# Optimization experiments

Hardware: AMD Instinct MI355X
Metric: run time of the kernel (lower is better)

The kernel has to match this reference:

```python
import jax, jax.numpy as jnp
import numpy as np

N_OPS = 8
TEMP = 1.0
EXP_CLIP = 10.0
EPS = 1e-6
# mask so that the 'none' primitive contributes exactly zero (including its bias term)
BIAS_MASK = jnp.array([0., 1., 1., 1., 1., 1., 1., 1.], dtype=jnp.float32)


def prim_feats(x):
    # x: [B, n_in] -> [B, n_in, K] primitive features
    # protected exp/ln/reciprocal to keep values finite (matches linear_clamp intent in fit())
    return jnp.stack([
        jnp.zeros_like(x),                      # none
        x,                                      # linear
        x * x,                                  # power_two
        x * x * x,                              # power_three
        jnp.exp(jnp.clip(x, -EXP_CLIP, EXP_CLIP)),  # exp
        jnp.log(jnp.abs(x) + EPS),              # ln
        x / (x * x + EPS),                      # reciprocal
        jnp.sin(x),                             # sin
    ], axis=-1)


def darts_layer(x, alphas, scale, bias):
    # alphas/scale/bias: [n_in, n_out, K]; x: [B, n_in]
    w = jax.nn.softmax(alphas / TEMP, axis=-1)          # softmax gating per (i,j)
    feats = prim_feats(x)                               # [B, n_in, K]
    out = jnp.einsum('bik,ijk->bj', feats, w * scale)   # gated sum over inputs and ops
    out = out + jnp.sum(w * bias * BIAS_MASK, axis=(0, 2))
    return out


def setup_inputs() -> dict:
    key = jax.random.key(0)
    ks = jax.random.split(key, 10)
    B, d0, d1, d2, dout, K = 16384, 512, 512, 512, 256, N_OPS
    ir, cs = 0.001, 0.1  # alpha init_range, coefficient scale
    x = jax.random.uniform(ks[0], (B, d0), dtype=jnp.float32) * 2.0 + 0.5
    alphas0 = ir * jax.random.normal(ks[1], (d0, d1, K), dtype=jnp.float32)
    scale0 = cs * jax.random.normal(ks[2], (d0, d1, K), dtype=jnp.float32)
    bias0 = cs * jax.random.normal(ks[3], (d0, d1, K), dtype=jnp.float32)
    alphas1 = ir * jax.random.normal(ks[4], (d1, d2, K), dtype=jnp.float32)
    scale1 = cs * jax.random.normal(ks[5], (d1, d2, K), dtype=jnp.float32)
    bias1 = cs * jax.random.normal(ks[6], (d1, d2, K), dtype=jnp.float32)
    W = jax.random.normal(ks[7], (dout, d2), dtype=jnp.float32) * (1.0 / np.sqrt(d2))
    b = jax.random.normal(ks[8], (dout, 1), dtype=jnp.float32) * 0.01
    return {"x": x, "alphas0": alphas0, "scale0": scale0, "bias0": bias0,
            "alphas1": alphas1, "scale1": scale1, "bias1": bias1, "W": W, "b": b}


def reference(x, alphas0, scale0, bias0, alphas1, scale1, bias1, W, b):
    h = darts_layer(x, alphas0, scale0, bias0)   # [B, 512]
    h = darts_layer(h, alphas1, scale1, bias1)   # [B, 512]
    out = h @ W.T + b.T                          # LinearDARTSLayer: [B, 256]
    return out
```

## Files before the change

### kernel.cpp

```cpp
#include <hip/hip_runtime.h>
#include <string.h>

typedef _Float16 f16x8 __attribute__((ext_vector_type(8)));
typedef float f32x4 __attribute__((ext_vector_type(4)));

#define EXP_CLIP 10.0f
#define FEPS 1e-6f
#define WSCALE 16384.0f
#define WDESCALE (1.0f/16384.0f)
#define PSCALE 1024.0f
#define PDESCALE (1.0f/1024.0f)

__device__ __forceinline__ _Float16 cvh(float v) {
  v = fminf(fmaxf(v, -60000.f), 60000.f);
  return (_Float16)v;
}

__device__ __forceinline__ void gload_lds16(const void* g, void* l) {
  __builtin_amdgcn_global_load_lds(
      (const __attribute__((address_space(1))) void*)g,
      (__attribute__((address_space(3))) void*)l, 16, 0, 0);
}

__device__ __forceinline__ int swz(int row, int colh) {
  return row * 64 + (colh ^ ((row & 7) << 3));
}

__device__ __forceinline__ float prim_eval(int kp, float x) {
  switch (kp) {
    case 0: return x;
    case 1: return x * x;
    case 2: return x * x * x;
    case 3: return __expf(fminf(fmaxf(x, -EXP_CLIP), EXP_CLIP));
    case 4: return __logf(fabsf(x) + FEPS);
    case 5: return x / (x * x + FEPS);
    default: return __sinf(x);
  }
}

__device__ __forceinline__ unsigned char enc_e5m2(float lo) {
  _Float16 lh = (_Float16)lo;
  unsigned short u;
  memcpy(&u, &lh, 2);
  unsigned t = (unsigned)u + 0x7Fu + ((u >> 8) & 1u);
  return (unsigned char)(t >> 8);
}

#define PIPE_TAIL() do { \
  __builtin_amdgcn_sched_barrier(0); \
  asm volatile("s_waitcnt vmcnt(0)" ::: "memory"); \
  __builtin_amdgcn_s_barrier(); \
  __builtin_amdgcn_sched_barrier(0); \
} while (0)

template <bool EMIT_LO>
__global__ __launch_bounds__(512)
void prep_weights(const float* __restrict__ alphas, const float* __restrict__ scale,
                  const float* __restrict__ bias, _Float16* __restrict__ Wh,
                  _Float16* __restrict__ Wl, float* __restrict__ biasvec) {
  int j = blockIdx.x;
  int i = threadIdx.x;
  size_t base = ((size_t)i * 512 + j) * 8;
  float a[8];
#pragma unroll
  for (int k = 0; k < 8; ++k) a[k] = alphas[base + k];
  float m = a[0];
#pragma unroll
  for (int k = 1; k < 8; ++k) m = fmaxf(m, a[k]);
  float e[8], sum = 0.f;
#pragma unroll
  for (int k = 0; k < 8; ++k) { e[k] = __expf(a[k] - m); sum += e[k]; }
  float inv = 1.f / sum;
  float bp = 0.f;
#pragma unroll
  for (int k = 1; k < 8; ++k) {
    float w = e[k] * inv;
    float ws = fminf(fmaxf(w * scale[base + k] * WSCALE, -60000.f), 60000.f);
    _Float16 wh = (_Float16)ws;
    size_t o = (size_t)j * 3584 + (size_t)(k - 1) * 512 + i;
    Wh[o] = wh;
    if (EMIT_LO) Wl[o] = (_Float16)(ws - (float)wh);
    bp += w * bias[base + k];
  }
  __shared__ float red[512];
  red[i] = bp;
  __syncthreads();
  for (int off = 256; off > 0; off >>= 1) {
    if (i < off) red[i] += red[i + off];
    __syncthreads();
  }
  if (i == 0) biasvec[j] = red[0];
}

__global__ __launch_bounds__(256)
void featurize_hilo(const float* __restrict__ in, _Float16* __restrict__ hi,
                    unsigned char* __restrict__ loB) {
  int t = blockIdx.x * 256 + threadIdx.x;
  int b = t >> 6, g = (t & 63) * 8;
  const float* xp = in + (size_t)b * 512 + g;
  float4 a = *(const float4*)xp;
  float4 c = *(const float4*)(xp + 4);
  float xv[8] = {a.x, a.y, a.z, a.w, c.x, c.y, c.z, c.w};
  _Float16* oh = hi + (size_t)b * 3584 + g;
  unsigned char* ol = loB + (size_t)b * 3584 + g;
#pragma unroll
  for (int kp = 0; kp < 7; ++kp) {
    f16x8 hv;
    unsigned long long lb = 0;
#pragma unroll
    for (int e = 0; e < 8; ++e) {
      float f = prim_eval(kp, xv[e]);
      _Float16 fh = (_Float16)f;
      hv[e] = fh;
      lb |= (unsigned long long)enc_e5m2(f - (float)fh) << (8 * e);
    }
    *(f16x8*)&oh[kp * 512] = hv;
    *(unsigned long long*)&ol[kp * 512] = lb;
  }
}

__global__ __launch_bounds__(256)
void featurize8(const float* __restrict__ in, _Float16* __restrict__ out) {
  int t = blockIdx.x * 256 + threadIdx.x;
  int b = t >> 6, g = (t & 63) * 8;
  const float* xp = in + (size_t)b * 512 + g;
  float4 a = *(const float4*)xp;
  float4 c = *(const float4*)(xp + 4);
  float xv[8] = {a.x, a.y, a.z, a.w, c.x, c.y, c.z, c.w};
  _Float16* o = out + (size_t)b * 3584 + g;
#pragma unroll
  for (int kp = 0; kp < 7; ++kp) {
    f16x8 v;
#pragma unroll
    for (int e = 0; e < 8; ++e) v[e] = cvh(prim_eval(kp, xv[e]));
    *(f16x8*)&o[kp * 512] = v;
  }
}

__global__ __launch_bounds__(256)
void cvt_half_k(const float* __restrict__ in, _Float16* __restrict__ out, int n) {
  int idx = blockIdx.x * 256 + threadIdx.x;
  if (idx < n) out[idx] = (_Float16)(in[idx] * PSCALE);
}

__global__ __launch_bounds__(256)
void gemm_l1_pre(const _Float16* __restrict__ Fhi, const unsigned char* __restrict__ FloB,
                 const _Float16* __restrict__ Wh, const _Float16* __restrict__ Wl,
                 const float* __restrict__ bias, float* __restrict__ H) {
  __shared__ __align__(16) _Float16 AhS[128 * 64];
  __shared__ __align__(16) unsigned char AlB[128 * 64];
  __shared__ __align__(16) _Float16 BhS[128 * 64];
  __shared__ __align__(16) _Float16 BlS[128 * 64];
  const int K = 3584;
  int lin = blockIdx.x;
  int wg = (lin & 7) * 64 + (lin >> 3);
  int bn = wg & 3, bm = wg >> 2;
  int row0 = bm * 128, col0 = bn * 128;
  int tid = threadIdx.x, lane = tid & 63, wave = tid >> 6;
  int wm = wave >> 1, wn = wave & 1;
  int l16 = lane & 15, lh = lane >> 4;
  int sr = lane >> 3, sc = ((lane & 7) * 8) ^ (sr << 3);
  int br = lane >> 2, bp_ = lane & 3;
  int bcs = (bp_ ^ ((br >> 1) & 3)) * 16;

  f32x4 acc[4][4];
#pragma unroll
  for (int m = 0; m < 4; ++m)
#pragma unroll
    for (int n = 0; n < 4; ++n) acc[m][n] = (f32x4){0.f, 0.f, 0.f, 0.f};

  for (int kk0 = 0; kk0 < K; kk0 += 64) {
    const _Float16* Agh = Fhi + (size_t)row0 * K + kk0;
    const unsigned char* Agl = FloB + (size_t)row0 * K + kk0;
    const _Float16* Bgh = Wh + (size_t)col0 * K + kk0;
    const _Float16* Bgl = Wl + (size_t)col0 * K + kk0;
#pragma unroll
    for (int it = 0; it < 4; ++it) {
      int chunk = it * 4 + wave;
      int r = chunk * 8 + sr;
      size_t go = (size_t)r * K + sc;
      gload_lds16(Agh + go, AhS + chunk * 512);
      gload_lds16(Bgh + go, BhS + chunk * 512);
      gload_lds16(Bgl + go, BlS + chunk * 512);
    }
#pragma unroll
    for (int it = 0; it < 2; ++it) {
      int chunk = it * 4 + wave;
      int r = chunk * 16 + br;
      gload_lds16(Agl + (size_t)r * K + bcs, AlB + chunk * 1024);
    }
    __syncthreads();
#pragma unroll
    for (int kc = 0; kc < 2; ++kc) {
      f16x8 ah[4], al[4];
#pragma unroll
      for (int m = 0; m < 4; ++m) {
        int row = wm * 64 + m * 16 + l16;
        ah[m] = *(const f16x8*)&AhS[swz(row, kc * 32 + lh * 8)];
        int cbyte = (kc * 32 + lh * 8) ^ (((row >> 1) & 3) << 4);
        uint2 d = *(const uint2*)&AlB[row * 64 + cbyte];
        union { unsigned u[4]; f16x8 v; } ex;
        ex.u[0] = ((d.x << 8) & 0xFF00u) | ((d.x << 16) & 0xFF000000u);
        ex.u[1] = ((d.x >> 8) & 0xFF00u) | (d.x & 0xFF000000u);
        ex.u[2] = ((d.y << 8) & 0xFF00u) | ((d.y << 16) & 0xFF000000u);
        ex.u[3] = ((d.y >> 8) & 0xFF00u) | (d.y & 0xFF000000u);
        al[m] = ex.v;
      }
#pragma unroll
      for (int n = 0; n < 4; ++n) {
        int ob = swz(wn * 64 + n * 16 + l16, kc * 32 + lh * 8);
        f16x8 bh = *(const f16x8*)&BhS[ob];
        f16x8 bl = *(const f16x8*)&BlS[ob];
#pragma unroll
        for (int m = 0; m < 4; ++m) {
          acc[m][n] = __builtin_amdgcn_mfma_f32_16x16x32_f16(ah[m], bh, acc[m][n], 0, 0, 0);
          acc[m][n] = __builtin_amdgcn_mfma_f32_16x16x32_f16(al[m], bh, acc[m][n], 0, 0, 0);
          acc[m][n] = __builtin_amdgcn_mfma_f32_16x16x32_f16(ah[m], bl, acc[m][n], 0, 0, 0);
        }
      }
    }
    __syncthreads();
  }

#pragma unroll
  for (int m = 0; m < 4; ++m) {
    int row = row0 + wm * 64 + m * 16 + lh * 4;
#pragma unroll
    for (int n = 0; n < 4; ++n) {
      int col = col0 + wn * 64 + n * 16 + l16;
      float bv = bias[col];
#pragma unroll
      for (int r = 0; r < 4; ++r)
        H[(size_t)(row + r) * 512 + col] = acc[m][n][r] * WDESCALE + bv;
    }
  }
}

template <bool OUT_HALF>
__global__ __launch_bounds__(512, 4)
void gemm_tn_pipe(const _Float16* __restrict__ A, const _Float16* __restrict__ BT,
                  const float* __restrict__ bias, void* __restrict__ C,
                  int M, int N, int K, int nbn_log2, int nwg, float outscale) {
  __shared__ __align__(16) _Float16 Ash[2][128 * 64];
  __shared__ __align__(16) _Float16 Bsh[2][128 * 64];
  int NT = K >> 6;
  int lin = blockIdx.x;
  int q = nwg >> 3;
  int wg = (lin & 7) * q + (lin >> 3);
  int bn = wg & ((1 << nbn_log2) - 1);
  int bm = wg >> nbn_log2;
  int row0 = bm * 128, col0 = bn * 128;
  int tid = threadIdx.x, lane = tid & 63, wave = tid >> 6;
  int wm = wave >> 2, wn = wave & 3;
  int l16 = lane & 15, lh = lane >> 4;
  int sr = lane >> 3, sc = ((lane & 7) * 8) ^ (sr << 3);

  const _Float16* Ag = A + (size_t)row0 * K;
  const _Float16* Bg = BT + (size_t)col0 * K;

  f32x4 acc[4][2];
#pragma unroll
  for (int m = 0; m < 4; ++m)
#pragma unroll
    for (int n = 0; n < 2; ++n) acc[m][n] = (f32x4){0.f, 0.f, 0.f, 0.f};

  auto stage = [&](int t, int p) {
    int kk = t * 64;
#pragma unroll
    for (int it = 0; it < 2; ++it) {
      int chunk = it * 8 + wave;
      int r = chunk * 8 + sr;
      size_t go = (size_t)r * K + kk + sc;
      gload_lds16(Ag + go, &Ash[p][chunk * 512]);
      gload_lds16(Bg + go, &Bsh[p][chunk * 512]);
    }
  };

  stage(0, 0);
  PIPE_TAIL();

#pragma unroll 1
  for (int t = 0; t < NT; ++t) {
    int p = t & 1;
    if (t + 1 < NT) stage(t + 1, p ^ 1);
    __builtin_amdgcn_sched_barrier(0);
    __builtin_amdgcn_s_setprio(1);
#pragma unroll
    for (int kc = 0; kc < 2; ++kc) {
      f16x8 af[4], bf[2];
#pragma unroll
      for (int m = 0; m < 4; ++m)
        af[m] = *(const f16x8*)&Ash[p][swz(wm * 64 + m * 16 + l16, kc * 32 + lh * 8)];
#pragma unroll
      for (int n = 0; n < 2; ++n)
        bf[n] = *(const f16x8*)&Bsh[p][swz(wn * 32 + n * 16 + l16, kc * 32 + lh * 8)];
#pragma unroll
      for (int n = 0; n < 2; ++n)
#pragma unroll
        for (int m = 0; m < 4; ++m)
          acc[m][n] = __builtin_amdgcn_mfma_f32_16x16x32_f16(af[m], bf[n], acc[m][n], 0, 0, 0);
    }
    __builtin_amdgcn_s_setprio(0);
    PIPE_TAIL();
  }

#pragma unroll
  for (int m = 0; m < 4; ++m) {
    int row = row0 + wm * 64 + m * 16 + lh * 4;
#pragma unroll
    for (int n = 0; n < 2; ++n) {
      int col = col0 + wn * 32 + n * 16 + l16;
      float bv = bias[col];
#pragma unroll
      for (int r = 0; r < 4; ++r) {
        float v = acc[m][n][r] * outscale + bv;
        if (OUT_HALF)
          ((_Float16*)C)[(size_t)(row + r) * N + col] = cvh(v);
        else
          ((float*)C)[(size_t)(row + r) * N + col] = v;
      }
    }
  }
}

__global__ __launch_bounds__(256, 2)
void gemm_l1_fused(const float* __restrict__ X, const _Float16* __restrict__ Wh,
                   const _Float16* __restrict__ Wl, const float* __restrict__ bias,
                   float* __restrict__ H) {
  __shared__ __align__(16) _Float16 AhS[128 * 64];
  __shared__ __align__(16) _Float16 AlS[128 * 64];
  __shared__ __align__(16) _Float16 BhS[128 * 64];
  __shared__ __align__(16) _Float16 BlS[128 * 64];
  const int K = 3584;
  int lin = blockIdx.x;
  int wg = (lin & 7) * 64 + (lin >> 3);
  int bn = wg & 3, bm = wg >> 2;
  int row0 = bm * 128, col0 = bn * 128;
  int tid = threadIdx.x, lane = tid & 63, wave = tid >> 6;
  int wm = wave >> 1, wn = wave & 1;
  int l16 = lane & 15, lh = lane >> 4;
  int sr = lane >> 3, sc = ((lane & 7) * 8) ^ (sr << 3);
  int ar = tid >> 3, ac = (tid & 7) * 8;

  f32x4 acc[4][4];
#pragma unroll
  for (int m = 0; m < 4; ++m)
#pragma unroll
    for (int n = 0; n < 4; ++n) acc[m][n] = (f32x4){0.f, 0.f, 0.f, 0.f};

#pragma unroll 1
  for (int kk0 = 0; kk0 < K; kk0 += 64) {
    int kp = kk0 >> 9, i0 = kk0 & 511;
    const _Float16* Bgh = Wh + (size_t)col0 * K + kk0;
    const _Float16* Bgl = Wl + (size_t)col0 * K + kk0;
#pragma unroll
    for (int it = 0; it < 4; ++it) {
      int chunk = it * 4 + wave;
      int r = chunk * 8 + sr;
      gload_lds16(Bgh + (size_t)r * K + sc, BhS + chunk * 512);
      gload_lds16(Bgl + (size_t)r * K + sc, BlS + chunk * 512);
    }
#pragma unroll
    for (int it = 0; it < 4; ++it) {
      int r = it * 32 + ar;
      const float* xp = X + (size_t)(row0 + r) * 512 + i0 + ac;
      float4 x01 = *(const float4*)xp;
      float4 x23 = *(const float4*)(xp + 4);
      float xv[8] = {x01.x, x01.y, x01.z, x01.w, x23.x, x23.y, x23.z, x23.w};
      f16x8 hv, lv;
#pragma unroll
      for (int e = 0; e < 8; ++e) {
        float f = prim_eval(kp, xv[e]);
        _Float16 fh = (_Float16)f;
        hv[e] = fh;
        lv[e] = (_Float16)(f - (float)fh);
      }
      int wo = swz(r, ac);
      *(f16x8*)&AhS[wo] = hv;
      *(f16x8*)&AlS[wo] = lv;
    }
    __syncthreads();
#pragma unroll
    for (int kc = 0; kc < 2; ++kc) {
      f16x8 ah[4], al[4];
#pragma unroll
      for (int m = 0; m < 4; ++m) {
        int off = swz(wm * 64 + m * 16 + l16, kc * 32 + lh * 8);
        ah[m] = *(const f16x8*)&AhS[off];
        al[m] = *(const f16x8*)&AlS[off];
      }
#pragma unroll
      for (int n = 0; n < 4; ++n) {
        int ob = swz(wn * 64 + n * 16 + l16, kc * 32 + lh * 8);
        f16x8 bh = *(const f16x8*)&BhS[ob];
        f16x8 bl = *(const f16x8*)&BlS[ob];
#pragma unroll
        for (int m = 0; m < 4; ++m) {
          acc[m][n] = __builtin_amdgcn_mfma_f32_16x16x32_f16(ah[m], bh, acc[m][n], 0, 0, 0);
          acc[m][n] = __builtin_amdgcn_mfma_f32_16x16x32_f16(al[m], bh, acc[m][n], 0, 0, 0);
          acc[m][n] = __builtin_amdgcn_mfma_f32_16x16x32_f16(ah[m], bl, acc[m][n], 0, 0, 0);
        }
      }
    }
    __syncthreads();
  }

#pragma unroll
  for (int m = 0; m < 4; ++m) {
    int row = row0 + wm * 64 + m * 16 + lh * 4;
#pragma unroll
    for (int n = 0; n < 4; ++n) {
      int col = col0 + wn * 64 + n * 16 + l16;
      float bv = bias[col];
#pragma unroll
      for (int r = 0; r < 4; ++r)
        H[(size_t)(row + r) * 512 + col] = acc[m][n][r] * WDESCALE + bv;
    }
  }
}

template <bool OUT_HALF>
__global__ __launch_bounds__(256)
void gemm_tn(const _Float16* __restrict__ A, const _Float16* __restrict__ BT,
             const float* __restrict__ bias, void* __restrict__ C,
             int M, int N, int K, int nbn_log2, int nwg, float outscale) {
  __shared__ __align__(16) _Float16 Ash[128 * 64];
  __shared__ __align__(16) _Float16 Bsh[128 * 64];
  int lin = blockIdx.x;
  int q = nwg >> 3;
  int wg = (lin & 7) * q + (lin >> 3);
  int bn = wg & ((1 << nbn_log2) - 1);
  int bm = wg >> nbn_log2;
  int row0 = bm * 128, col0 = bn * 128;
  int tid = threadIdx.x, lane = tid & 63, wave = tid >> 6;
  int wm = wave >> 1, wn = wave & 1;
  int l16 = lane & 15, lh = lane >> 4;
  int sr = lane >> 3;
  int sc = ((lane & 7) * 8) ^ (sr << 3);

  f32x4 acc[4][4];
#pragma unroll
  for (int m = 0; m < 4; ++m)
#pragma unroll
    for (int n = 0; n < 4; ++n) acc[m][n] = (f32x4){0.f, 0.f, 0.f, 0.f};

  for (int kk0 = 0; kk0 < K; kk0 += 64) {
    const _Float16* Ag = A + (size_t)row0 * K + kk0;
    const _Float16* Bg = BT + (size_t)col0 * K + kk0;
#pragma unroll
    for (int it = 0; it < 4; ++it) {
      int chunk = it * 4 + wave;
      int r = chunk * 8 + sr;
      gload_lds16(Ag + (size_t)r * K + sc, Ash + chunk * 512);
      gload_lds16(Bg + (size_t)r * K + sc, Bsh + chunk * 512);
    }
    __syncthreads();
#pragma unroll
    for (int kc = 0; kc < 2; ++kc) {
      f16x8 af[4], bf[4];
#pragma unroll
      for (int m = 0; m < 4; ++m)
        af[m] = *(const f16x8*)&Ash[swz(wm * 64 + m * 16 + l16, kc * 32 + lh * 8)];
#pragma unroll
      for (int n = 0; n < 4; ++n)
        bf[n] = *(const f16x8*)&Bsh[swz(wn * 64 + n * 16 + l16, kc * 32 + lh * 8)];
#pragma unroll
      for (int m = 0; m < 4; ++m)
#pragma unroll
        for (int n = 0; n < 4; ++n)
          acc[m][n] = __builtin_amdgcn_mfma_f32_16x16x32_f16(af[m], bf[n], acc[m][n], 0, 0, 0);
    }
    __syncthreads();
  }

#pragma unroll
  for (int m = 0; m < 4; ++m) {
    int row = row0 + wm * 64 + m * 16 + lh * 4;
#pragma unroll
    for (int n = 0; n < 4; ++n) {
      int col = col0 + wn * 64 + n * 16 + l16;
      float bv = bias[col];
#pragma unroll
      for (int r = 0; r < 4; ++r) {
        float v = acc[m][n][r] * outscale + bv;
        if (OUT_HALF)
          ((_Float16*)C)[(size_t)(row + r) * N + col] = cvh(v);
        else
          ((float*)C)[(size_t)(row + r) * N + col] = v;
      }
    }
  }
}

extern "C" void kernel_launch(void* const* d_in, const int* in_sizes, int n_in,
                              void* d_out, int out_size, void* d_ws, size_t ws_size,
                              hipStream_t stream) {
  const float* x  = (const float*)d_in[0];
  const float* a0 = (const float*)d_in[1];
  const float* s0 = (const float*)d_in[2];
  const float* b0 = (const float*)d_in[3];
  const float* a1 = (const float*)d_in[4];
  const float* s1 = (const float*)d_in[5];
  const float* b1 = (const float*)d_in[6];
  const float* W  = (const float*)d_in[7];
  const float* bb = (const float*)d_in[8];

  const int Bn = 16384, D = 512, KK = 3584, DOUT = 256;
  const size_t szF  = (size_t)Bn * KK * 2;
  const size_t szFb = (size_t)Bn * KK;
  const size_t szH  = (size_t)Bn * D * 4;
  const size_t szW  = (size_t)D * KK * 2;
  const size_t szP  = (size_t)DOUT * D * 2;
  const size_t needA = szF + szFb + szH + 3 * szW + szP + 4096;

  if (ws_size >= needA) {
    char* p = (char*)d_ws;
    _Float16*      Fhi  = (_Float16*)p; p += szF;
    unsigned char* FloB = (unsigned char*)p; p += szFb;
    float*    h     = (float*)p;
    _Float16* ghalf = (_Float16*)p; p += szH;
    _Float16* Wh0   = (_Float16*)p; p += szW;
    _Float16* Wl0   = (_Float16*)p; p += szW;
    _Float16* Wh1   = (_Float16*)p; p += szW;
    _Float16* WpT   = (_Float16*)p; p += szP;
    float*    biasv = (float*)p;

    prep_weights<true ><<<dim3(512), dim3(512), 0, stream>>>(a0, s0, b0, Wh0, Wl0, biasv);
    prep_weights<false><<<dim3(512), dim3(512), 0, stream>>>(a1, s1, b1, Wh1, nullptr, biasv + 512);
    cvt_half_k<<<dim3(512), dim3(256), 0, stream>>>(W, WpT, DOUT * D);

    featurize_hilo<<<dim3(Bn * 64 / 256), dim3(256), 0, stream>>>(x, Fhi, FloB);
    gemm_l1_pre<<<dim3(512), dim3(256), 0, stream>>>(Fhi, FloB, Wh0, Wl0, biasv, h);

    featurize8<<<dim3(Bn * 64 / 256), dim3(256), 0, stream>>>(h, Fhi);
    gemm_tn_pipe<true><<<dim3(512), dim3(512), 0, stream>>>(Fhi, Wh1, biasv + 512, ghalf,
                                                            Bn, D, KK, 2, 512, WDESCALE);

    gemm_tn_pipe<false><<<dim3(256), dim3(512), 0, stream>>>(ghalf, WpT, bb, (float*)d_out,
                                                             Bn, DOUT, D, 1, 256, PDESCALE);
  } else {
    char* p = (char*)d_ws;
    _Float16* Afeat = (_Float16*)p;
    _Float16* Wh0   = (_Float16*)p;
    _Float16* Wl0   = (_Float16*)(p + szW);
    p += szF;
    float*    h     = (float*)p;
    _Float16* ghalf = (_Float16*)p;
    p += szH;
    _Float16* Wh1   = (_Float16*)p; p += szW;
    _Float16* WpT   = (_Float16*)p; p += szP;
    float*    biasv = (float*)p;

    prep_weights<true ><<<dim3(512), dim3(512), 0, stream>>>(a0, s0, b0, Wh0, Wl0, biasv);
    prep_weights<false><<<dim3(512), dim3(512), 0, stream>>>(a1, s1, b1, Wh1, nullptr, biasv + 512);
    cvt_half_k<<<dim3(512), dim3(256), 0, stream>>>(W, WpT, DOUT * D);

    gemm_l1_fused<<<dim3(512), dim3(256), 0, stream>>>(x, Wh0, Wl0, biasv, h);

    featurize8<<<dim3(Bn * 64 / 256), dim3(256), 0, stream>>>(h, Afeat);
    gemm_tn<true><<<dim3(512), dim3(256), 0, stream>>>(Afeat, Wh1, biasv + 512, ghalf,
                                                       Bn, D, KK, 2, 512, WDESCALE);

    gemm_tn<false><<<dim3(256), dim3(256), 0, stream>>>(ghalf, WpT, bb, (float*)d_out,
                                                        Bn, DOUT, D, 1, 256, PDESCALE);
  }
}
```

Before: 331.4 us.

## Software-pipeline layer-1 split-precision GEMM with triple-buffered LDS stages

Replaces the single-buffered 64-wide K loop of the first-layer hi/lo GEMM with a 32-wide K loop that keeps three LDS stages for A-hi, A-lo and B-hi and two for B-lo. Global-to-LDS loads for upcoming tiles are issued before the MFMAs on the current tile, and the wait uses partial vmcnt counts followed by a raw s_barrier. It also raises wave priority around the MFMA block and uses new swizzle patterns for the narrower tiles. The goal is to hide global-load latency behind matrix math, at the cost of more barriers per K and delicate vmcnt bookkeeping.

```diff
diff --git a/kernel.cpp b/kernel.cpp
--- a/kernel.cpp
+++ b/kernel.cpp
@@ -144,14 +144,14 @@
 }
 
 __global__ __launch_bounds__(256)
-void gemm_l1_pre(const _Float16* __restrict__ Fhi, const unsigned char* __restrict__ FloB,
-                 const _Float16* __restrict__ Wh, const _Float16* __restrict__ Wl,
-                 const float* __restrict__ bias, float* __restrict__ H) {
-  __shared__ __align__(16) _Float16 AhS[128 * 64];
-  __shared__ __align__(16) unsigned char AlB[128 * 64];
-  __shared__ __align__(16) _Float16 BhS[128 * 64];
-  __shared__ __align__(16) _Float16 BlS[128 * 64];
-  const int K = 3584;
+void gemm_l1_p3(const _Float16* __restrict__ Fhi, const unsigned char* __restrict__ FloB,
+                const _Float16* __restrict__ Wh, const _Float16* __restrict__ Wl,
+                const float* __restrict__ bias, float* __restrict__ H) {
+  __shared__ __align__(16) _Float16 AhS[3][128 * 32];
+  __shared__ __align__(16) unsigned char AlBs[3][128 * 32];
+  __shared__ __align__(16) _Float16 BhS[3][128 * 32];
+  __shared__ __align__(16) _Float16 BlS[2][128 * 32];
+  const int K = 3584, NT = 112;
   int lin = blockIdx.x;
   int wg = (lin & 7) * 64 + (lin >> 3);
   int bn = wg & 3, bm = wg >> 2;
@@ -159,9 +159,21 @@
   int tid = threadIdx.x, lane = tid & 63, wave = tid >> 6;
   int wm = wave >> 1, wn = wave & 1;
   int l16 = lane & 15, lh = lane >> 4;
-  int sr = lane >> 3, sc = ((lane & 7) * 8) ^ (sr << 3);
-  int br = lane >> 2, bp_ = lane & 3;
-  int bcs = (bp_ ^ ((br >> 1) & 3)) * 16;
+
+  int mr = lane >> 2;
+  int msh = ((lane & 3) ^ ((mr & 3) ^ ((mr >> 2) & 3))) * 8;
+  int ar2 = lane >> 1;
+  int acs = ((lane & 1) ^ ((lane >> 3) & 1)) * 16;
+
+  int xA = (l16 & 3) ^ ((l16 >> 2) & 3);
+  int xb = (l16 >> 2) & 1;
+  int colA = (lh ^ xA) * 8;
+  int colB = (((lh >> 1) ^ xb) * 16) + (lh & 1) * 8;
+
+  const _Float16* Agh = Fhi + (size_t)row0 * K;
+  const unsigned char* Agl = FloB + (size_t)row0 * K;
+  const _Float16* Bgh = Wh + (size_t)col0 * K;
+  const _Float16* Bgl = Wl + (size_t)col0 * K;
 
   f32x4 acc[4][4];
 #pragma unroll
@@ -169,36 +181,53 @@
 #pragma unroll
     for (int n = 0; n < 4; ++n) acc[m][n] = (f32x4){0.f, 0.f, 0.f, 0.f};
 
-  for (int kk0 = 0; kk0 < K; kk0 += 64) {
-    const _Float16* Agh = Fhi + (size_t)row0 * K + kk0;
-    const unsigned char* Agl = FloB + (size_t)row0 * K + kk0;
-    const _Float16* Bgh = Wh + (size_t)col0 * K + kk0;
-    const _Float16* Bgl = Wl + (size_t)col0 * K + kk0;
-#pragma unroll
-    for (int it = 0; it < 4; ++it) {
-      int chunk = it * 4 + wave;
-      int r = chunk * 8 + sr;
-      size_t go = (size_t)r * K + sc;
-      gload_lds16(Agh + go, AhS + chunk * 512);
-      gload_lds16(Bgh + go, BhS + chunk * 512);
-      gload_lds16(Bgl + go, BlS + chunk * 512);
-    }
+  auto stage_main = [&](int t, int c) {
+    size_t kk = (size_t)t * 32;
 #pragma unroll
     for (int it = 0; it < 2; ++it) {
       int chunk = it * 4 + wave;
-      int r = chunk * 16 + br;
-      gload_lds16(Agl + (size_t)r * K + bcs, AlB + chunk * 1024);
-    }
-    __syncthreads();
-#pragma unroll
-    for (int kc = 0; kc < 2; ++kc) {
+      int r = chunk * 16 + mr;
+      size_t go = (size_t)r * K + kk + msh;
+      gload_lds16(Agh + go, &AhS[c][chunk * 512]);
+      gload_lds16(Bgh + go, &BhS[c][chunk * 512]);
+    }
+    {
+      int r = wave * 32 + ar2;
+      gload_lds16(Agl + (size_t)r * K + kk + acs, &AlBs[c][wave * 1024]);
+    }
+  };
+  auto stage_bl = [&](int t, int p) {
+    size_t kk = (size_t)t * 32;
+#pragma unroll
+    for (int it = 0; it < 2; ++it) {
+      int chunk = it * 4 + wave;
+      int r = chunk * 16 + mr;
+      gload_lds16(Bgl + (size_t)r * K + kk + msh, &BlS[p][chunk * 512]);
+    }
+  };
+
+  stage_bl(0, 0);
+  stage_main(0, 0);
+  stage_main(1, 1);
+  __builtin_amdgcn_sched_barrier(0);
+  asm volatile("s_waitcnt vmcnt(5)" ::: "memory");
+  __builtin_amdgcn_s_barrier();
+  __builtin_amdgcn_sched_barrier(0);
+
+  int c0 = 0, c2 = 2;
+#pragma unroll 1
+  for (int t = 0; t < NT; ++t) {
+    if (t + 1 < NT) stage_bl(t + 1, (t + 1) & 1);
+    if (t + 2 < NT) stage_main(t + 2, c2);
+    __builtin_amdgcn_sched_barrier(0);
+    __builtin_amdgcn_s_setprio(1);
+    {
       f16x8 ah[4], al[4];
 #pragma unroll
       for (int m = 0; m < 4; ++m) {
         int row = wm * 64 + m * 16 + l16;
-        ah[m] = *(const f16x8*)&AhS[swz(row, kc * 32 + lh * 8)];
-        int cbyte = (kc * 32 + lh * 8) ^ (((row >> 1) & 3) << 4);
-        uint2 d = *(const uint2*)&AlB[row * 64 + cbyte];
+        ah[m] = *(const f16x8*)&AhS[c0][row * 32 + colA];
+        uint2 d = *(const uint2*)&AlBs[c0][row * 32 + colB];
         union { unsigned u[4]; f16x8 v; } ex;
         ex.u[0] = ((d.x << 8) & 0xFF00u) | ((d.x << 16) & 0xFF000000u);
         ex.u[1] = ((d.x >> 8) & 0xFF00u) | (d.x & 0xFF000000u);
@@ -208,9 +237,9 @@
       }
 #pragma unroll
       for (int n = 0; n < 4; ++n) {
-        int ob = swz(wn * 64 + n * 16 + l16, kc * 32 + lh * 8);
-        f16x8 bh = *(const f16x8*)&BhS[ob];
-        f16x8 bl = *(const f16x8*)&BlS[ob];
+        int rowb = wn * 64 + n * 16 + l16;
+        f16x8 bh = *(const f16x8*)&BhS[c0][rowb * 32 + colA];
+        f16x8 bl = *(const f16x8*)&BlS[t & 1][rowb * 32 + colA];
 #pragma unroll
         for (int m = 0; m < 4; ++m) {
           acc[m][n] = __builtin_amdgcn_mfma_f32_16x16x32_f16(ah[m], bh, acc[m][n], 0, 0, 0);
@@ -219,7 +248,17 @@
         }
       }
     }
-    __syncthreads();
+    __builtin_amdgcn_s_setprio(0);
+    __builtin_amdgcn_sched_barrier(0);
+    if (t + 2 < NT) {
+      asm volatile("s_waitcnt vmcnt(5)" ::: "memory");
+    } else {
+      asm volatile("s_waitcnt vmcnt(0)" ::: "memory");
+    }
+    __builtin_amdgcn_s_barrier();
+    __builtin_amdgcn_sched_barrier(0);
+    c0 = (c0 == 2) ? 0 : c0 + 1;
+    c2 = (c2 == 2) ? 0 : c2 + 1;
   }
 
 #pragma unroll
@@ -530,7 +569,7 @@
     cvt_half_k<<<dim3(512), dim3(256), 0, stream>>>(W, WpT, DOUT * D);
 
     featurize_hilo<<<dim3(Bn * 64 / 256), dim3(256), 0, stream>>>(x, Fhi, FloB);
-    gemm_l1_pre<<<dim3(512), dim3(256), 0, stream>>>(Fhi, FloB, Wh0, Wl0, biasv, h);
+    gemm_l1_p3<<<dim3(512), dim3(256), 0, stream>>>(Fhi, FloB, Wh0, Wl0, biasv, h);
 
     featurize8<<<dim3(Bn * 64 / 256), dim3(256), 0, stream>>>(h, Fhi);
     gemm_tn_pipe<true><<<dim3(512), dim3(512), 0, stream>>>(Fhi, Wh1, biasv + 512, ghalf,
```

Result: slower. 367.6 us (+10.9%).
